# Optimization experiments

Hardware: AMD Instinct MI355X
Metric: run time of the kernel (lower is better)

Reference implementation:

```python
import jax, jax.numpy as jnp
import numpy as np

B, S, D, H = 8, 512, 1024, 16
DH = D // H
GAMMA = 0.1      # kl_gamma
KL_EPS = 1e-10
LN_EPS = 1e-5
SCALE = 1.0 / np.sqrt(DH).astype(np.float32)


def setup_inputs() -> dict:
    key = jax.random.key(0)
    ks = iter(jax.random.split(key, 32))
    rnd = lambda shape, s: jax.random.normal(next(ks), shape, jnp.float32) * s
    inp = {
        'title_features': rnd((B, S, D), 1.0),
        'content_features': rnd((B, S, D), 1.0),
    }
    for pre in ('t2c', 'c2t'):
        # small Q/K weights + bias 1.0 keep row-means of scores positive (log is defined)
        inp[pre + '_wq'] = rnd((D, D), 0.02); inp[pre + '_bq'] = jnp.ones((D,), jnp.float32)
        inp[pre + '_wk'] = rnd((D, D), 0.02); inp[pre + '_bk'] = jnp.ones((D,), jnp.float32)
        inp[pre + '_wv'] = rnd((D, D), 0.02); inp[pre + '_bv'] = jnp.zeros((D,), jnp.float32)
        inp[pre + '_wo'] = rnd((D, D), 0.02); inp[pre + '_bo'] = jnp.zeros((D,), jnp.float32)
    inp['gate_w'] = rnd((2 * D, D), 0.02)
    inp['gate_b'] = jnp.zeros((D,), jnp.float32)
    inp['ln_g'] = jnp.ones((D,), jnp.float32)
    inp['ln_b'] = jnpps = jnp.zeros((D,), jnp.float32)
    inp['ln_b'] = jnp.zeros((D,), jnp.float32)
    return inp


def _daa(q_in, k_in, v_in, wq, bq, wk, bk, wv, bv, wo, bo):
    """DivergenceAlignedAttention forward (eval mode, use_uniform_target=False)."""
    Bq, Sq, _ = q_in.shape
    Sk = k_in.shape[1]
    Q = (q_in @ wq + bq).reshape(Bq, Sq, H, DH)
    K = (k_in @ wk + bk).reshape(Bq, Sk, H, DH)
    V = (v_in @ wv + bv).reshape(Bq, Sk, H, DH)
    scores = jnp.einsum('bqhd,bkhd->bhqk', Q, K) * SCALE           # [B,H,Sq,Sk]
    tgt = jnp.mean(scores, axis=-1, keepdims=True)                 # row mean
    scores = scores + GAMMA * jnp.log(tgt + KL_EPS)                # fused KL term
    attn = jax.nn.softmax(scores, axis=-1)
    ctx = jnp.einsum('bhqk,bkhd->bqhd', attn, V).reshape(Bq, Sq, D)
    return ctx @ wo + bo


def _layer_norm(x, g, b):
    mu = jnp.mean(x, axis=-1, keepdims=True)
    var = jnp.mean(jnp.square(x - mu), axis=-1, keepdims=True)
    return g * (x - mu) / jnp.sqrt(var + LN_EPS) + b


def reference(title_features, content_features,
              t2c_wq, t2c_bq, t2c_wk, t2c_bk, t2c_wv, t2c_bv, t2c_wo, t2c_bo,
              c2t_wq, c2t_bq, c2t_wk, c2t_bk, c2t_wv, c2t_bv, c2t_wo, c2t_bo,
              gate_w, gate_b, ln_g, ln_b):
    t2c = _daa(content_features, title_features, title_features,
               t2c_wq, t2c_bq, t2c_wk, t2c_bk, t2c_wv, t2c_bv, t2c_wo, t2c_bo)
    c2t = _daa(title_features, content_features, content_features,
               c2t_wq, c2t_bq, c2t_wk, c2t_bk, c2t_wv, c2t_bv, c2t_wo, c2t_bo)
    gate_t = jax.nn.sigmoid(jnp.concatenate([title_features, t2c], axis=-1) @ gate_w + gate_b)
    gate_c = jax.nn.sigmoid(jnp.concatenate([content_features, c2t], axis=-1) @ gate_w + gate_b)
    fused_title = _layer_norm(gate_t * title_features + (1.0 - gate_t) * t2c, ln_g, ln_b)
    fused_content = _layer_norm(gate_c * content_features + (1.0 - gate_c) * c2t, ln_g, ln_b)
    return (fused_title, fused_content)
```

## Files before the change

### kernel.cpp

```cpp
#include <hip/hip_runtime.h>
#include <cstdint>
#include <cstddef>

typedef unsigned short ushort_t;
typedef unsigned int u32;
typedef __attribute__((ext_vector_type(8))) short bf16x8;
typedef __attribute__((ext_vector_type(4))) short bf16x4;
typedef __attribute__((ext_vector_type(4))) float f32x4;
typedef __attribute__((ext_vector_type(4))) unsigned short u16x4;

#define DEV static __device__ __forceinline__

DEV ushort_t f2bf(float f) {
  u32 x = __float_as_uint(f);
  x += 0x7fff + ((x >> 16) & 1);
  return (ushort_t)(x >> 16);
}
DEV float bf2f(ushort_t u) { return __uint_as_float(((u32)u) << 16); }

DEV u32 cvtpk(float a, float b) {
  u32 r;
  asm("v_cvt_pk_bf16_f32 %0, %1, %2" : "=v"(r) : "v"(a), "v"(b));
  return r;
}

DEV void gload16(const ushort_t* g, ushort_t* l) {
  __builtin_amdgcn_global_load_lds(
      (const __attribute__((address_space(1))) void*)g,
      (__attribute__((address_space(3))) void*)l, 16, 0, 0);
}


__global__ __launch_bounds__(256) void cvt_inputs(
    const float* __restrict__ xa, const float* __restrict__ xb,
    ushort_t* __restrict__ oa, ushort_t* __restrict__ ob) {
  int i = blockIdx.x * 256 + threadIdx.x;
  f32x4 va = ((const f32x4*)xa)[i];
  f32x4 vb = ((const f32x4*)xb)[i];
  u16x4 ua, ub;
#pragma unroll
  for (int j = 0; j < 4; ++j) { ua[j] = f2bf(va[j]); ub[j] = f2bf(vb[j]); }
  ((u16x4*)oa)[i] = ua;
  ((u16x4*)ob)[i] = ub;
}

struct Src11 { const float* p[11]; };

__global__ __launch_bounds__(256) void transpose_cvt(
    Src11 srcs, ushort_t* __restrict__ WTall, ushort_t* __restrict__ WgT,
    ushort_t* __restrict__ WoBF) {
  const int z = blockIdx.z;
  if (z != 8 && blockIdx.y >= 32) return;
  const float* src = srcs.p[z];
  int tx = threadIdx.x & 31, ty = threadIdx.x >> 5;
  int n0 = blockIdx.x << 5, k0 = blockIdx.y << 5;
  if (z >= 9) {
    ushort_t* dst = WoBF + ((size_t)(z - 9) << 20);
#pragma unroll
    for (int i = 0; i < 4; ++i) {
      size_t off = (size_t)(k0 + ty + i * 8) * 1024 + n0 + tx;
      dst[off] = f2bf(src[off]);
    }
    return;
  }
  const int K = (z == 8) ? 2048 : 1024;
  ushort_t* dst = (z == 8) ? WgT : WTall + ((size_t)z << 20);
  __shared__ float t[32][33];
#pragma unroll
  for (int i = 0; i < 4; ++i)
    t[ty + i * 8][tx] = src[(size_t)(k0 + ty + i * 8) * 1024 + n0 + tx];
  __syncthreads();
#pragma unroll
  for (int i = 0; i < 4; ++i)
    dst[(size_t)(n0 + ty + i * 8) * K + k0 + tx] = f2bf(t[tx][ty + i * 8]);
}

__global__ __launch_bounds__(256) void gb2_kernel(
    const float* __restrict__ bo0, const float* __restrict__ bo1,
    const ushort_t* __restrict__ WgT, float* __restrict__ gb2) {
  const int wgl = blockIdx.x * 4 + (threadIdx.x >> 6);
  const int lane = threadIdx.x & 63;
  const int dir = wgl >> 10, n = wgl & 1023;
  const float* bo = dir ? bo1 : bo0;
  const ushort_t* wrow = WgT + ((size_t)n << 11) + 1024 + (lane << 4);
  float s = 0.f;
#pragma unroll
  for (int j = 0; j < 16; ++j) s += bo[(lane << 4) + j] * bf2f(wrow[j]);
#pragma unroll
  for (int d = 1; d < 64; d <<= 1) s += __shfl_xor(s, d, 64);
  if (lane == 0) gb2[wgl] = s;
}

__global__ __launch_bounds__(256, 3) void gemm_wp(
    const ushort_t* __restrict__ WgT, const ushort_t* __restrict__ WoBF,
    ushort_t* __restrict__ WpT) {
  __shared__ ushort_t As[128 * 64];
  __shared__ ushort_t Bs[128 * 64];
  const int tid = threadIdx.x;
  const int w = tid >> 6, lane = tid & 63;
  const int g = lane >> 4, c = lane & 15;
  const int wm = (w >> 1) << 6, wn = (w & 1) << 6;
  const int m0 = blockIdx.x << 7, n0 = blockIdx.y << 7;
  const int group = m0 >> 10;
  const int csw = (lane & 7) ^ (lane >> 3);

  f32x4 acc[4][4];
#pragma unroll
  for (int i = 0; i < 4; ++i)
#pragma unroll
    for (int j = 0; j < 4; ++j) acc[i][j] = f32x4{0.f, 0.f, 0.f, 0.f};

  for (int k0 = 0; k0 < 1024; k0 += 64) {
#pragma unroll
    for (int i = 0; i < 4; ++i) {
      const int chunk = (w << 2) + i;
      const int row = (chunk << 3) + (lane >> 3);
      gload16(WgT + ((size_t)((m0 + row) & 1023) << 11) + 1024 + k0 + (csw << 3),
              &As[(size_t)chunk << 9]);
      gload16(WoBF + ((size_t)group << 20) + ((size_t)(n0 + row) << 10) + k0 + (csw << 3),
              &Bs[(size_t)chunk << 9]);
    }
    __syncthreads();
    const int cg = c & 7;
#pragma unroll
    for (int ks = 0; ks < 2; ++ks) {
      bf16x8 af[4], bfr[4];
#pragma unroll
      for (int mi = 0; mi < 4; ++mi)
        af[mi] = *(const bf16x8*)&As[((wm + mi * 16 + c) << 6) +
                                     ((((ks << 2) | g) ^ cg) << 3)];
#pragma unroll
      for (int ni = 0; ni < 4; ++ni)
        bfr[ni] = *(const bf16x8*)&Bs[((wn + ni * 16 + c) << 6) +
                                      ((((ks << 2) | g) ^ cg) << 3)];
#pragma unroll
      for (int mi = 0; mi < 4; ++mi)
#pragma unroll
        for (int ni = 0; ni < 4; ++ni)
          acc[mi][ni] = __builtin_amdgcn_mfma_f32_16x16x32_bf16(
              af[mi], bfr[ni], acc[mi][ni], 0, 0, 0);
    }
    __syncthreads();
  }
#pragma unroll
  for (int ni = 0; ni < 4; ++ni) {
    const int n = n0 + wn + ni * 16 + c;
#pragma unroll
    for (int mi = 0; mi < 4; ++mi) {
      const int mb = m0 + wm + mi * 16 + (g << 2);
      f32x4 a = acc[mi][ni];
#pragma unroll
      for (int r = 0; r < 4; ++r)
        WpT[((size_t)group << 20) + ((size_t)((mb + r) & 1023) << 10) + n] = f2bf(a[r]);
    }
  }
}

enum { M_QKVG = 0, M_OG = 1 };
struct Bias8 { const float* p[8]; };

template <int MODE>
__global__ __launch_bounds__(256, 3) void gemm_kernel(
    const ushort_t* __restrict__ Aa, const ushort_t* __restrict__ Ab,
    const ushort_t* __restrict__ WTall, const ushort_t* __restrict__ WgT,
    const ushort_t* __restrict__ WpT, Bias8 bt, const float* __restrict__ gb2,
    ushort_t* __restrict__ outQ, ushort_t* __restrict__ gt) {
  __shared__ ushort_t smem[16384];
  ushort_t* As = smem;
  ushort_t* Bs = smem + 8192;
  const int tid = threadIdx.x;
  const int w = tid >> 6, lane = tid & 63;
  const int g = lane >> 4, c = lane & 15;
  const int wm = (w >> 1) << 6, wn = (w & 1) << 6;
  const int bid = (int)blockIdx.x;
  const int xcd = bid & 7, idx = bid >> 3;
  const int mt = (xcd << 3) + (idx & 7), nt = idx >> 3;
  const int m0 = mt << 7, n0 = nt << 7;
  const int group = m0 >> 12;
  const int nch = n0 >> 10;
  const int csw = (lane & 7) ^ (lane >> 3);

  const ushort_t* Asrc = (MODE == M_QKVG)
      ? ((group ? Ab : Aa) + ((size_t)(m0 & 4095) << 10))
      : (Aa + ((size_t)group << 22) + ((size_t)(m0 & 4095) << 6));

  const ushort_t* Bb;
  int bstr, bidx = -1;
  if (MODE == M_QKVG) {
    if (nch < 3) {
      bidx = group * 3 + nch;
      Bb = WTall + ((size_t)bidx << 20) + ((size_t)(n0 & 1023) << 10);
      bstr = 1024;
    } else {
      Bb = WgT + ((size_t)(n0 & 1023) << 11);
      bstr = 2048;
    }
  } else {
    if (nch == 0) {
      Bb = WTall + ((size_t)(6 + group) << 20) + ((size_t)n0 << 10);
      bstr = 1024;
    } else {
      Bb = WpT + ((size_t)group << 20) + ((size_t)(n0 & 1023) << 10);
      bstr = 1024;
    }
  }

  f32x4 acc[4][4];
#pragma unroll
  for (int i = 0; i < 4; ++i)
#pragma unroll
    for (int j = 0; j < 4; ++j) acc[i][j] = f32x4{0.f, 0.f, 0.f, 0.f};

  for (int k0 = 0; k0 < 1024; k0 += 64) {
#pragma unroll
    for (int i = 0; i < 4; ++i) {
      const int chunk = (w << 2) + i;
      const int row = (chunk << 3) + (lane >> 3);
      const ushort_t* ap;
      if (MODE == M_QKVG)
        ap = Asrc + ((size_t)row << 10) + k0 + (csw << 3);
      else
        ap = Asrc + ((size_t)(k0 >> 6) << 18) + ((size_t)row << 6) + (csw << 3);
      gload16(ap, &As[(size_t)chunk << 9]);
      gload16(Bb + (size_t)row * bstr + k0 + (csw << 3), &Bs[(size_t)chunk << 9]);
    }
    __syncthreads();
    const int cg = c & 7;
#pragma unroll
    for (int ks = 0; ks < 2; ++ks) {
      bf16x8 af[4], bfr[4];
#pragma unroll
      for (int mi = 0; mi < 4; ++mi)
        af[mi] = *(const bf16x8*)&As[((wm + mi * 16 + c) << 6) +
                                     ((((ks << 2) | g) ^ cg) << 3)];
#pragma unroll
      for (int ni = 0; ni < 4; ++ni)
        bfr[ni] = *(const bf16x8*)&Bs[((wn + ni * 16 + c) << 6) +
                                      ((((ks << 2) | g) ^ cg) << 3)];
#pragma unroll
      for (int mi = 0; mi < 4; ++mi)
#pragma unroll
        for (int ni = 0; ni < 4; ++ni)
          acc[mi][ni] = __builtin_amdgcn_mfma_f32_16x16x32_bf16(
              af[mi], bfr[ni], acc[mi][ni], 0, 0, 0);
    }
    __syncthreads();
  }

  const bool vt_path = (MODE == M_QKVG) && (nch < 3) && (bidx == 1 || bidx == 5);
  if (vt_path) {
#pragma unroll
    for (int ni = 0; ni < 4; ++ni) {
      const int nloc = (n0 + wn + ni * 16 + c) & 1023;
      const float bv = bt.p[bidx][nloc];
      const int h = nloc >> 6, d = nloc & 63;
#pragma unroll
      for (int mi = 0; mi < 4; ++mi) {
        const int mrow = (m0 + wm + mi * 16 + (g << 2)) & 4095;
        const int b = mrow >> 9, s = mrow & 511;
        f32x4 a = acc[mi][ni];
        u16x4 o;
#pragma unroll
        for (int r = 0; r < 4; ++r) o[r] = f2bf(a[r] + bv);
        *(u16x4*)&outQ[((size_t)bidx << 22) +
                       (((size_t)((b * 16 + h) * 64 + d)) << 9) + s] = o;
      }
    }
  } else {
#pragma unroll
    for (int ni = 0; ni < 4; ++ni) {
      const int col = wn + ni * 16 + c;
      const int nloc = (n0 + col) & 1023;
      float bv;
      if (MODE == M_QKVG)
        bv = (nch < 3) ? bt.p[bidx][nloc]
                       : bt.p[6][nloc] + gb2[(group << 10) + nloc];
      else
        bv = (nch == 0) ? bt.p[group][nloc] : 0.f;
#pragma unroll
      for (int mi = 0; mi < 4; ++mi) {
        const int rowb = wm + mi * 16 + (g << 2);
        f32x4 a = acc[mi][ni];
#pragma unroll
        for (int r = 0; r < 4; ++r)
          smem[((rowb + r) << 7) + col] = f2bf(a[r] + bv);
      }
    }
    __syncthreads();
    const int lr = tid >> 4;
    const int lc = (tid & 15) << 3;
    ushort_t* obase;
    size_t rbase;
    if (MODE == M_QKVG) {
      if (nch < 3) { obase = outQ + ((size_t)bidx << 22); rbase = (size_t)(m0 & 4095); }
      else         { obase = gt;                          rbase = (size_t)m0; }
    } else {
      if (nch == 0) { obase = outQ; rbase = (size_t)m0; }
      else          { obase = gt;   rbase = (size_t)m0; }
    }
    const int ncol = (n0 & 1023) + lc;
#pragma unroll
    for (int j = 0; j < 8; ++j) {
      const int row = (j << 4) + lr;
      bf16x8 v = *(const bf16x8*)&smem[(row << 7) + lc];
      *(bf16x8*)&obase[((rbase + row) << 10) + ncol] = v;
    }
  }
}

__global__ __launch_bounds__(256, 4) void attn_kernel(
    const ushort_t* __restrict__ QKV, ushort_t* __restrict__ ctx) {
  __shared__ ushort_t Ks[2][4096];
  __shared__ ushort_t Vs[2][4096];
  const int tid = threadIdx.x, w = tid >> 6, lane = tid & 63;
  const int g = lane >> 4, c = lane & 15, c7 = c & 7;
  const int bid = (int)blockIdx.x;
  const int wid = (bid & 7) * 256 + (bid >> 3);
  const int dir = wid >> 10;
  const int bh = (wid >> 3) & 127, qt = wid & 7;
  const int b = bh >> 4, h = bh & 15;
  const int q0 = (qt << 6) + (w << 4);
  const int qs = dir ? 2 : 3, kslot = dir ? 4 : 0, vslot = dir ? 5 : 1;
  const ushort_t* Qb = QKV + ((size_t)qs << 22) + (((size_t)b << 9) << 10) + (h << 6);
  const ushort_t* Kb = QKV + ((size_t)kslot << 22) + (((size_t)b << 9) << 10) + (h << 6);
  const ushort_t* Vb = QKV + ((size_t)vslot << 22) + ((size_t)bh << 15);

  auto stageK = [&](int bb, int kc) {
#pragma unroll
    for (int i = 0; i < 2; ++i) {
      int idx = tid + (i << 8);
      int r = idx >> 3, sl = idx & 7;
      int cs = sl ^ (r & 7);
      gload16(Kb + ((size_t)((kc << 6) + r) << 10) + (cs << 3), &Ks[bb][idx << 3]);
    }
  };
  auto stageV = [&](int bb, int vc) {
#pragma unroll
    for (int i = 0; i < 2; ++i) {
      int idx = tid + (i << 8);
      int r = idx >> 3, sl = idx & 7;
      int cs = sl ^ (r & 7);
      gload16(Vb + ((size_t)r << 9) + (vc << 6) + (cs << 3), &Vs[bb][idx << 3]);
    }
  };

  bf16x8 qf0 = *(const bf16x8*)&Qb[((size_t)(q0 + c) << 10) + (g << 3)];
  bf16x8 qf1 = *(const bf16x8*)&Qb[((size_t)(q0 + c) << 10) + 32 + (g << 3)];

  const float SC = 0.125f;
  float m = -1e30f, sum = 0.f;
  f32x4 pacc[4];
#pragma unroll
  for (int dt = 0; dt < 4; ++dt) pacc[dt] = f32x4{0.f, 0.f, 0.f, 0.f};

  stageK(0, 0);
  stageV(0, 0);
  __syncthreads();

#pragma unroll
  for (int cc = 0; cc < 8; ++cc) {
    const int buf = cc & 1;
    if (cc < 7) { stageK(buf ^ 1, cc + 1); stageV(buf ^ 1, cc + 1); }

    f32x4 st[4];
    __builtin_amdgcn_s_setprio(1);
#pragma unroll
    for (int t = 0; t < 4; ++t) {
      const ushort_t* base = &Ks[buf][((t << 4) + c) << 6];
      bf16x8 a0 = *(const bf16x8*)&base[(g ^ c7) << 3];
      bf16x8 a1 = *(const bf16x8*)&base[((4 | g) ^ c7) << 3];
      f32x4 z = {0.f, 0.f, 0.f, 0.f};
      z = __builtin_amdgcn_mfma_f32_16x16x32_bf16(a0, qf0, z, 0, 0, 0);
      z = __builtin_amdgcn_mfma_f32_16x16x32_bf16(a1, qf1, z, 0, 0, 0);
      st[t] = z;
    }
    __builtin_amdgcn_s_setprio(0);

    float mx = fmaxf(fmaxf(st[0][0], st[0][1]), fmaxf(st[0][2], st[0][3]));
#pragma unroll
    for (int t = 1; t < 4; ++t)
      mx = fmaxf(mx, fmaxf(fmaxf(st[t][0], st[t][1]), fmaxf(st[t][2], st[t][3])));
    mx = fmaxf(mx, __shfl_xor(mx, 16, 64));
    mx = fmaxf(mx, __shfl_xor(mx, 32, 64));
    const float mn = fmaxf(m, mx);
    const float scale = __expf((m - mn) * SC);
    m = mn;
    float ls = 0.f;
#pragma unroll
    for (int t = 0; t < 4; ++t)
#pragma unroll
      for (int r = 0; r < 4; ++r) {
        float p = __expf((st[t][r] - mn) * SC);
        st[t][r] = p;
        ls += p;
      }
    ls += __shfl_xor(ls, 16, 64);
    ls += __shfl_xor(ls, 32, 64);
    sum = sum * scale + ls;
#pragma unroll
    for (int dt = 0; dt < 4; ++dt)
#pragma unroll
      for (int r = 0; r < 4; ++r) pacc[dt][r] *= scale;

#pragma unroll
    for (int ks = 0; ks < 4; ++ks) {
      union { bf16x4 v; u32 wd[2]; } pb;
      pb.wd[0] = cvtpk(st[ks][0], st[ks][1]);
      pb.wd[1] = cvtpk(st[ks][2], st[ks][3]);
      __builtin_amdgcn_s_setprio(1);
#pragma unroll
      for (int dt = 0; dt < 4; ++dt) {
        const int slot = ((ks << 1) | (g >> 1)) ^ c7;
        bf16x4 av = *(const bf16x4*)
            &Vs[buf][(((dt << 4) + c) << 6) + (slot << 3) + ((g & 1) << 2)];
        asm("v_mfma_f32_16x16x16_bf16 %0, %1, %2, %0"
            : "+v"(pacc[dt]) : "v"(av), "v"(pb.v));
      }
      __builtin_amdgcn_s_setprio(0);
    }
    __syncthreads();
  }

  const float inv = 1.0f / sum;
  ushort_t* cb = ctx + ((size_t)dir << 22) + ((size_t)h << 18) +
                 ((size_t)(b * 512 + q0 + c) << 6);
#pragma unroll
  for (int dt = 0; dt < 4; ++dt) {
    union { u16x4 o; u32 wd[2]; } ou;
    ou.wd[0] = cvtpk(pacc[dt][0] * inv, pacc[dt][1] * inv);
    ou.wd[1] = cvtpk(pacc[dt][2] * inv, pacc[dt][3] * inv);
    *(u16x4*)&cb[(dt << 4) + (g << 2)] = ou.o;
  }
}

__global__ __launch_bounds__(256) void fuse_ln(
    const float* __restrict__ xt, const float* __restrict__ xc,
    const ushort_t* __restrict__ ao, const ushort_t* __restrict__ gt,
    const ushort_t* __restrict__ gp,
    const float* __restrict__ lng, const float* __restrict__ lnb,
    float* __restrict__ out) {
  const int row = blockIdx.x, dir = row >> 12, r = row & 4095;
  const float* x = (dir ? xc : xt) + ((size_t)r << 10);
  const ushort_t* a = ao + ((size_t)row << 10);
  const ushort_t* g1 = gt + ((size_t)row << 10);
  const ushort_t* g2 = gp + ((size_t)row << 10);
  float* o = out + ((size_t)row << 10);
  const int t = threadIdx.x, w = t >> 6, lane = t & 63;
  f32x4 xv = ((const f32x4*)x)[t];
  u16x4 av = ((const u16x4*)a)[t];
  u16x4 gv = ((const u16x4*)g1)[t];
  u16x4 pv = ((const u16x4*)g2)[t];
  f32x4 f;
  float sm = 0.f, sq = 0.f;
#pragma unroll
  for (int j = 0; j < 4; ++j) {
    float gate = 1.f / (1.f + __expf(-(bf2f(gv[j]) + bf2f(pv[j]))));
    float fv = gate * xv[j] + (1.f - gate) * bf2f(av[j]);
    f[j] = fv; sm += fv; sq += fv * fv;
  }
#pragma unroll
  for (int d = 1; d < 64; d <<= 1) {
    sm += __shfl_xor(sm, d, 64);
    sq += __shfl_xor(sq, d, 64);
  }
  __shared__ float ps[8];
  if (lane == 0) { ps[w] = sm; ps[4 + w] = sq; }
  __syncthreads();
  sm = ps[0] + ps[1] + ps[2] + ps[3];
  sq = ps[4] + ps[5] + ps[6] + ps[7];
  const float mu = sm * (1.f / 1024.f);
  const float var = sq * (1.f / 1024.f) - mu * mu;
  const float rstd = rsqrtf(var + 1e-5f);
  f32x4 lg = ((const f32x4*)lng)[t], lb = ((const f32x4*)lnb)[t];
  f32x4 ov;
#pragma unroll
  for (int j = 0; j < 4; ++j) ov[j] = lg[j] * (f[j] - mu) * rstd + lb[j];
  ((f32x4*)o)[t] = ov;
}

extern "C" void kernel_launch(void* const* d_in, const int* in_sizes, int n_in,
                              void* d_out, int out_size, void* d_ws, size_t ws_size,
                              hipStream_t stream) {
  (void)in_sizes; (void)n_in; (void)out_size; (void)ws_size;
  const float* title = (const float*)d_in[0];
  const float* content = (const float*)d_in[1];

  char* ws = (char*)d_ws;
  const size_t MB = 1u << 20;
  ushort_t* Xt    = (ushort_t*)(ws + 0 * MB);
  ushort_t* Xc    = (ushort_t*)(ws + 8 * MB);
  ushort_t* ctx   = (ushort_t*)(ws + 0 * MB);
  ushort_t* WTall = (ushort_t*)(ws + 16 * MB);
  ushort_t* WgT   = (ushort_t*)(ws + 32 * MB);
  ushort_t* QKV   = (ushort_t*)(ws + 36 * MB);
  ushort_t* ao    = (ushort_t*)(ws + 36 * MB);
  ushort_t* gpart = (ushort_t*)(ws + 52 * MB);
  ushort_t* gt    = (ushort_t*)(ws + 84 * MB);
  ushort_t* WoBF  = (ushort_t*)(ws + 100 * MB);
  ushort_t* WpT   = (ushort_t*)(ws + 104 * MB);
  float*    gb2   = (float*)   (ws + 108 * MB);

  cvt_inputs<<<4096, 256, 0, stream>>>(title, content, Xt, Xc);

  Src11 srcs;
  srcs.p[0] = (const float*)d_in[4];  srcs.p[1] = (const float*)d_in[6];
  srcs.p[2] = (const float*)d_in[10]; srcs.p[3] = (const float*)d_in[2];
  srcs.p[4] = (const float*)d_in[12]; srcs.p[5] = (const float*)d_in[14];
  srcs.p[6] = (const float*)d_in[8];  srcs.p[7] = (const float*)d_in[16];
  srcs.p[8] = (const float*)d_in[18];
  srcs.p[9] = (const float*)d_in[8];  srcs.p[10] = (const float*)d_in[16];
  transpose_cvt<<<dim3(32, 64, 11), 256, 0, stream>>>(srcs, WTall, WgT, WoBF);

  gb2_kernel<<<512, 256, 0, stream>>>((const float*)d_in[9], (const float*)d_in[17],
                                      WgT, gb2);
  gemm_wp<<<dim3(16, 8), 256, 0, stream>>>(WgT, WoBF, WpT);

  Bias8 bq;
  bq.p[0] = (const float*)d_in[5];  bq.p[1] = (const float*)d_in[7];
  bq.p[2] = (const float*)d_in[11]; bq.p[3] = (const float*)d_in[3];
  bq.p[4] = (const float*)d_in[13]; bq.p[5] = (const float*)d_in[15];
  bq.p[6] = (const float*)d_in[19]; bq.p[7] = nullptr;
  gemm_kernel<M_QKVG><<<2048, 256, 0, stream>>>(Xt, Xc, WTall, WgT, WpT, bq, gb2,
                                                QKV, gt);

  attn_kernel<<<2048, 256, 0, stream>>>(QKV, ctx);

  Bias8 bo;
  bo.p[0] = (const float*)d_in[9]; bo.p[1] = (const float*)d_in[17];
  for (int i = 2; i < 8; ++i) bo.p[i] = nullptr;
  gemm_kernel<M_OG><<<1024, 256, 0, stream>>>(ctx, nullptr, WTall, WgT, WpT, bo, gb2,
                                              ao, gpart);

  fuse_ln<<<8192, 256, 0, stream>>>(title, content, ao, gt, gpart,
                                    (const float*)d_in[20], (const float*)d_in[21],
                                    (float*)d_out);
}
```

Before: 220.3 us.

## Process two query tiles per wave in attention and skip rescale conditionally

Each attention block now covers 128 query rows instead of 64, with every wave handling two 16-row query tiles that share the staged K and V chunks. The grid is halved, which cuts K/V global loads and LDS staging per query. The online softmax now rescales the accumulators only when the running max grows by more than a threshold, so most iterations skip that multiply. In exchange each wave holds roughly twice as many registers, which may lower occupancy, and the fewer blocks may fill the GPU less evenly.

```diff
diff --git a/kernel.cpp b/kernel.cpp
--- a/kernel.cpp
+++ b/kernel.cpp
@@ -315,11 +315,11 @@
   const int tid = threadIdx.x, w = tid >> 6, lane = tid & 63;
   const int g = lane >> 4, c = lane & 15, c7 = c & 7;
   const int bid = (int)blockIdx.x;
-  const int wid = (bid & 7) * 256 + (bid >> 3);
-  const int dir = wid >> 10;
-  const int bh = (wid >> 3) & 127, qt = wid & 7;
+  const int wid = (bid & 7) * 128 + (bid >> 3);
+  const int dir = wid >> 9;
+  const int bh = (wid >> 2) & 127, qt = wid & 3;
   const int b = bh >> 4, h = bh & 15;
-  const int q0 = (qt << 6) + (w << 4);
+  const int q0 = (qt << 7) + (w << 4);
   const int qs = dir ? 2 : 3, kslot = dir ? 4 : 0, vslot = dir ? 5 : 1;
   const ushort_t* Qb = QKV + ((size_t)qs << 22) + (((size_t)b << 9) << 10) + (h << 6);
   const ushort_t* Kb = QKV + ((size_t)kslot << 22) + (((size_t)b << 9) << 10) + (h << 6);
@@ -344,14 +344,19 @@
     }
   };
 
-  bf16x8 qf0 = *(const bf16x8*)&Qb[((size_t)(q0 + c) << 10) + (g << 3)];
-  bf16x8 qf1 = *(const bf16x8*)&Qb[((size_t)(q0 + c) << 10) + 32 + (g << 3)];
+  bf16x8 qfA0 = *(const bf16x8*)&Qb[((size_t)(q0 + c) << 10) + (g << 3)];
+  bf16x8 qfA1 = *(const bf16x8*)&Qb[((size_t)(q0 + c) << 10) + 32 + (g << 3)];
+  bf16x8 qfB0 = *(const bf16x8*)&Qb[((size_t)(q0 + 64 + c) << 10) + (g << 3)];
+  bf16x8 qfB1 = *(const bf16x8*)&Qb[((size_t)(q0 + 64 + c) << 10) + 32 + (g << 3)];
 
   const float SC = 0.125f;
-  float m = -1e30f, sum = 0.f;
-  f32x4 pacc[4];
-#pragma unroll
-  for (int dt = 0; dt < 4; ++dt) pacc[dt] = f32x4{0.f, 0.f, 0.f, 0.f};
+  float mA = -1e30f, sumA = 0.f, mB = -1e30f, sumB = 0.f;
+  f32x4 paccA[4], paccB[4];
+#pragma unroll
+  for (int dt = 0; dt < 4; ++dt) {
+    paccA[dt] = f32x4{0.f, 0.f, 0.f, 0.f};
+    paccB[dt] = f32x4{0.f, 0.f, 0.f, 0.f};
+  }
 
   stageK(0, 0);
   stageV(0, 0);
@@ -362,51 +367,80 @@
     const int buf = cc & 1;
     if (cc < 7) { stageK(buf ^ 1, cc + 1); stageV(buf ^ 1, cc + 1); }
 
-    f32x4 st[4];
+    f32x4 stA[4], stB[4];
     __builtin_amdgcn_s_setprio(1);
 #pragma unroll
     for (int t = 0; t < 4; ++t) {
       const ushort_t* base = &Ks[buf][((t << 4) + c) << 6];
       bf16x8 a0 = *(const bf16x8*)&base[(g ^ c7) << 3];
       bf16x8 a1 = *(const bf16x8*)&base[((4 | g) ^ c7) << 3];
-      f32x4 z = {0.f, 0.f, 0.f, 0.f};
-      z = __builtin_amdgcn_mfma_f32_16x16x32_bf16(a0, qf0, z, 0, 0, 0);
-      z = __builtin_amdgcn_mfma_f32_16x16x32_bf16(a1, qf1, z, 0, 0, 0);
-      st[t] = z;
+      f32x4 zA = {0.f, 0.f, 0.f, 0.f}, zB = {0.f, 0.f, 0.f, 0.f};
+      zA = __builtin_amdgcn_mfma_f32_16x16x32_bf16(a0, qfA0, zA, 0, 0, 0);
+      zB = __builtin_amdgcn_mfma_f32_16x16x32_bf16(a0, qfB0, zB, 0, 0, 0);
+      zA = __builtin_amdgcn_mfma_f32_16x16x32_bf16(a1, qfA1, zA, 0, 0, 0);
+      zB = __builtin_amdgcn_mfma_f32_16x16x32_bf16(a1, qfB1, zB, 0, 0, 0);
+      stA[t] = zA;
+      stB[t] = zB;
     }
     __builtin_amdgcn_s_setprio(0);
 
-    float mx = fmaxf(fmaxf(st[0][0], st[0][1]), fmaxf(st[0][2], st[0][3]));
-#pragma unroll
-    for (int t = 1; t < 4; ++t)
-      mx = fmaxf(mx, fmaxf(fmaxf(st[t][0], st[t][1]), fmaxf(st[t][2], st[t][3])));
-    mx = fmaxf(mx, __shfl_xor(mx, 16, 64));
-    mx = fmaxf(mx, __shfl_xor(mx, 32, 64));
-    const float mn = fmaxf(m, mx);
-    const float scale = __expf((m - mn) * SC);
-    m = mn;
-    float ls = 0.f;
+    float mxA = fmaxf(fmaxf(stA[0][0], stA[0][1]), fmaxf(stA[0][2], stA[0][3]));
+    float mxB = fmaxf(fmaxf(stB[0][0], stB[0][1]), fmaxf(stB[0][2], stB[0][3]));
+#pragma unroll
+    for (int t = 1; t < 4; ++t) {
+      mxA = fmaxf(mxA, fmaxf(fmaxf(stA[t][0], stA[t][1]), fmaxf(stA[t][2], stA[t][3])));
+      mxB = fmaxf(mxB, fmaxf(fmaxf(stB[t][0], stB[t][1]), fmaxf(stB[t][2], stB[t][3])));
+    }
+    mxA = fmaxf(mxA, __shfl_xor(mxA, 16, 64));
+    mxB = fmaxf(mxB, __shfl_xor(mxB, 16, 64));
+    mxA = fmaxf(mxA, __shfl_xor(mxA, 32, 64));
+    mxB = fmaxf(mxB, __shfl_xor(mxB, 32, 64));
+    if (!__all(mxA <= mA + 64.f)) {
+      const float mn = fmaxf(mA, mxA);
+      const float sc = __expf((mA - mn) * SC);
+      mA = mn;
+      sumA *= sc;
+#pragma unroll
+      for (int dt = 0; dt < 4; ++dt)
+#pragma unroll
+        for (int r = 0; r < 4; ++r) paccA[dt][r] *= sc;
+    }
+    if (!__all(mxB <= mB + 64.f)) {
+      const float mn = fmaxf(mB, mxB);
+      const float sc = __expf((mB - mn) * SC);
+      mB = mn;
+      sumB *= sc;
+#pragma unroll
+      for (int dt = 0; dt < 4; ++dt)
+#pragma unroll
+        for (int r = 0; r < 4; ++r) paccB[dt][r] *= sc;
+    }
+    float lsA = 0.f, lsB = 0.f;
 #pragma unroll
     for (int t = 0; t < 4; ++t)
 #pragma unroll
       for (int r = 0; r < 4; ++r) {
-        float p = __expf((st[t][r] - mn) * SC);
-        st[t][r] = p;
-        ls += p;
+        float pA = __expf((stA[t][r] - mA) * SC);
+        float pB = __expf((stB[t][r] - mB) * SC);
+        stA[t][r] = pA;
+        stB[t][r] = pB;
+        lsA += pA;
+        lsB += pB;
       }
-    ls += __shfl_xor(ls, 16, 64);
-    ls += __shfl_xor(ls, 32, 64);
-    sum = sum * scale + ls;
-#pragma unroll
-    for (int dt = 0; dt < 4; ++dt)
-#pragma unroll
-      for (int r = 0; r < 4; ++r) pacc[dt][r] *= scale;
+    lsA += __shfl_xor(lsA, 16, 64);
+    lsB += __shfl_xor(lsB, 16, 64);
+    lsA += __shfl_xor(lsA, 32, 64);
+    lsB += __shfl_xor(lsB, 32, 64);
+    sumA += lsA;
+    sumB += lsB;
 
 #pragma unroll
     for (int ks = 0; ks < 4; ++ks) {
-      union { bf16x4 v; u32 wd[2]; } pb;
-      pb.wd[0] = cvtpk(st[ks][0], st[ks][1]);
-      pb.wd[1] = cvtpk(st[ks][2], st[ks][3]);
+      union { bf16x4 v; u32 wd[2]; } pbA, pbB;
+      pbA.wd[0] = cvtpk(stA[ks][0], stA[ks][1]);
+      pbA.wd[1] = cvtpk(stA[ks][2], stA[ks][3]);
+      pbB.wd[0] = cvtpk(stB[ks][0], stB[ks][1]);
+      pbB.wd[1] = cvtpk(stB[ks][2], stB[ks][3]);
       __builtin_amdgcn_s_setprio(1);
 #pragma unroll
       for (int dt = 0; dt < 4; ++dt) {
@@ -414,22 +448,29 @@
         bf16x4 av = *(const bf16x4*)
             &Vs[buf][(((dt << 4) + c) << 6) + (slot << 3) + ((g & 1) << 2)];
         asm("v_mfma_f32_16x16x16_bf16 %0, %1, %2, %0"
-            : "+v"(pacc[dt]) : "v"(av), "v"(pb.v));
+            : "+v"(paccA[dt]) : "v"(av), "v"(pbA.v));
+        asm("v_mfma_f32_16x16x16_bf16 %0, %1, %2, %0"
+            : "+v"(paccB[dt]) : "v"(av), "v"(pbB.v));
       }
       __builtin_amdgcn_s_setprio(0);
     }
     __syncthreads();
   }
 
-  const float inv = 1.0f / sum;
-  ushort_t* cb = ctx + ((size_t)dir << 22) + ((size_t)h << 18) +
-                 ((size_t)(b * 512 + q0 + c) << 6);
+  const float invA = 1.0f / sumA;
+  const float invB = 1.0f / sumB;
+  ushort_t* cbA = ctx + ((size_t)dir << 22) + ((size_t)h << 18) +
+                  ((size_t)(b * 512 + q0 + c) << 6);
+  ushort_t* cbB = cbA + ((size_t)64 << 6);
 #pragma unroll
   for (int dt = 0; dt < 4; ++dt) {
-    union { u16x4 o; u32 wd[2]; } ou;
-    ou.wd[0] = cvtpk(pacc[dt][0] * inv, pacc[dt][1] * inv);
-    ou.wd[1] = cvtpk(pacc[dt][2] * inv, pacc[dt][3] * inv);
-    *(u16x4*)&cb[(dt << 4) + (g << 2)] = ou.o;
+    union { u16x4 o; u32 wd[2]; } oa, ob;
+    oa.wd[0] = cvtpk(paccA[dt][0] * invA, paccA[dt][1] * invA);
+    oa.wd[1] = cvtpk(paccA[dt][2] * invA, paccA[dt][3] * invA);
+    ob.wd[0] = cvtpk(paccB[dt][0] * invB, paccB[dt][1] * invB);
+    ob.wd[1] = cvtpk(paccB[dt][2] * invB, paccB[dt][3] * invB);
+    *(u16x4*)&cbA[(dt << 4) + (g << 2)] = oa.o;
+    *(u16x4*)&cbB[(dt << 4) + (g << 2)] = ob.o;
   }
 }
 
@@ -523,7 +564,7 @@
   gemm_kernel<M_QKVG><<<2048, 256, 0, stream>>>(Xt, Xc, WTall, WgT, WpT, bq, gb2,
                                                 QKV, gt);
 
-  attn_kernel<<<2048, 256, 0, stream>>>(QKV, ctx);
+  attn_kernel<<<1024, 256, 0, stream>>>(QKV, ctx);
 
   Bias8 bo;
   bo.p[0] = (const float*)d_in[9]; bo.p[1] = (const float*)d_in[17];
```

Result: faster. 208.3 us (median of 3 runs) (-5.5%).
